# Optimization experiments

Hardware: AMD Instinct MI355X
Metric: run time of the kernel (lower is better)

The kernel has to match this reference:

```python
import jax, jax.numpy as jnp
import numpy as np

B, P, K, E, H, V, C = 128, 64, 64, 300, 300, 50000, 3


def lstm0(x, Wih, bih, bhh):
    # PyTorch LSTMCell single step with zero initial (h, c) state.
    # gates = x @ Wih^T + bih + Whh @ 0 + bhh ; chunks order: i, f, g, o
    g = x @ Wih.T + bih + bhh
    i, f, gg, o = jnp.split(g, 4, axis=-1)
    c = jax.nn.sigmoid(i) * jnp.tanh(gg)
    return jax.nn.sigmoid(o) * jnp.tanh(c)


def setup_inputs() -> dict:
    key = jax.random.key(0)
    ks = jax.random.split(key, 24)
    d = {}
    d["premise"] = jax.random.randint(ks[0], (B, P), 1, V)
    d["premise_len"] = jax.random.randint(ks[1], (B,), P // 2, P + 1)
    d["hypothesis"] = jax.random.randint(ks[2], (B, K), 1, V)
    d["hypothesis_len"] = jax.random.randint(ks[3], (B,), K // 2, K + 1)
    embed = jax.random.normal(ks[4], (V, E), jnp.float32) * 0.1
    d["embed"] = embed.at[0].set(0.0)  # padding_idx=0
    d["w_e"] = jax.random.uniform(ks[5], (H,), jnp.float32)
    xav = (2.0 / (H + H)) ** 0.5
    d["W_s"] = jax.random.normal(ks[6], (H, H), jnp.float32) * xav
    d["W_t"] = jax.random.normal(ks[7], (H, H), jnp.float32) * xav
    d["W_m"] = jax.random.normal(ks[8], (H, H), jnp.float32) * xav
    d["fc_w"] = jax.random.normal(ks[9], (C, H), jnp.float32) * (2.0 / (H + C)) ** 0.5
    d["fc_b"] = jax.random.uniform(ks[10], (C,), jnp.float32)
    s = 1.0 / np.sqrt(H)
    def cell(k1, k2, k3, k4, in_dim):
        return (jax.random.uniform(k1, (4 * H, in_dim), jnp.float32, -s, s),
                jax.random.uniform(k2, (4 * H, H), jnp.float32, -s, s),
                jax.random.uniform(k3, (4 * H,), jnp.float32, -s, s),
                jax.random.uniform(k4, (4 * H,), jnp.float32, -s, s))
    d["Wih_p"], d["Whh_p"], d["bih_p"], d["bhh_p"] = cell(ks[11], ks[12], ks[13], ks[14], E)
    d["Wih_h"], d["Whh_h"], d["bih_h"], d["bhh_h"] = cell(ks[15], ks[16], ks[17], ks[18], E)
    d["Wih_m"], d["Whh_m"], d["bih_m"], d["bhh_m"] = cell(ks[19], ks[20], ks[21], ks[22], 2 * H)
    return d


def reference(premise, premise_len, hypothesis, hypothesis_len, embed, w_e,
              W_s, W_t, W_m, fc_w, fc_b,
              Wih_p, Whh_p, bih_p, bhh_p,
              Wih_h, Whh_h, bih_h, bhh_h,
              Wih_m, Whh_m, bih_m, bhh_m):
    prem_emb = embed[premise]      # [B,P,E]
    hypo_emb = embed[hypothesis]   # [B,K,E]
    # Original code calls LSTMCell on a whole sequence -> per-token single step
    # with zero initial state (no temporal recurrence in these two cells).
    h_s = lstm0(prem_emb, Wih_p, bih_p, bhh_p)  # [B,P,H]
    h_t = lstm0(hypo_emb, Wih_h, bih_h, bhh_h)  # [B,K,H]
    s_proj = h_s @ W_s.T                         # [B,P,H]
    t_proj = jnp.transpose(h_t @ W_t.T, (1, 0, 2))  # [K,B,H]
    h_t_kb = jnp.transpose(h_t, (1, 0, 2))          # [K,B,H]
    b, p = h_s.shape[0], h_s.shape[1]
    pmask = jnp.arange(p)[None, :] < premise_len[:, None]  # [B,P]
    neg = jnp.finfo(s_proj.dtype).min

    def step(h_m, xs):
        t_k, ht_k = xs  # [B,H], [B,H]
        m_proj = h_m @ W_m.T  # [B,H]
        e = jnp.einsum('bph,h->bp',
                       jnp.tanh(s_proj + t_k[:, None, :] + m_proj[:, None, :]), w_e)
        e = jnp.where(pmask, e, neg)
        alpha = jax.nn.softmax(e, axis=1)           # softmax over valid premise pos
        a = jnp.einsum('bp,bph->bh', alpha, h_s)    # attention-weighted premise
        m = jnp.concatenate([a, ht_k], axis=-1)     # [B,2H]
        # lstm_match is re-invoked with zero state each k in the original
        h_m_new = lstm0(m, Wih_m, bih_m, bhh_m)
        return h_m_new, h_m_new

    _, hs_all = jax.lax.scan(step, jnp.zeros((b, s_proj.shape[-1]), s_proj.dtype),
                             (t_proj, h_t_kb))      # [K,B,H]
    h_fin = hs_all[hypothesis_len - 1, jnp.arange(b)]  # h_m at last valid hypo step
    logits = h_fin @ fc_w.T + fc_b
    return jax.nn.softmax(logits, axis=1)
```

## Files before the change

kernel.cpp:

```cpp
#include <hip/hip_runtime.h>
#include <stdint.h>

typedef unsigned short u16;
typedef __attribute__((ext_vector_type(8))) __bf16 bf16x8;
typedef __attribute__((ext_vector_type(4))) float f32x4;

__device__ __forceinline__ float bf2f(u16 u) {
    union { unsigned int i; float f; } v; v.i = ((unsigned int)u) << 16; return v.f;
}
__device__ __forceinline__ float bf2f_lo(unsigned int u) {
    union { unsigned int i; float f; } v; v.i = u << 16; return v.f;
}
__device__ __forceinline__ float bf2f_hi(unsigned int u) {
    union { unsigned int i; float f; } v; v.i = u & 0xffff0000u; return v.f;
}
__device__ __forceinline__ u16 f2bf(float f) {
    union { float f; unsigned int i; } v; v.f = f;
    unsigned int x = v.i;
    unsigned int r = (x + 0x7fffu + ((x >> 16) & 1u)) >> 16;
    return (u16)r;
}
__device__ __forceinline__ float rdf(const void* p, size_t i, int isbf) {
    return isbf ? bf2f(((const u16*)p)[i]) : ((const float*)p)[i];
}
__device__ __forceinline__ float fast_sigmoid(float x) {
    return __builtin_amdgcn_rcpf(1.f + __expf(-x));
}
__device__ __forceinline__ float fast_tanh(float x) {
    float u = __expf(x + x);
    return 1.f - 2.f * __builtin_amdgcn_rcpf(u + 1.f);
}
__device__ __forceinline__ bf16x8 as_bf8(uint4 u) {
    union { uint4 a; bf16x8 b; } c; c.a = u; return c.b;
}

#define BB 128
#define PP 64
#define KK 64
#define HH 300
#define MROWS 8192
#define KPAD 320
#define N3H 900
#define GLD 912
#define NT1 19
#define NT4 57

__global__ void detect_dtype(const u16* __restrict__ raw, int* __restrict__ flag) {
    __shared__ int cnt;
    if (threadIdx.x == 0) cnt = 0;
    __syncthreads();
    if (threadIdx.x < 300 && (raw[threadIdx.x] & 0x8000u)) atomicAdd(&cnt, 1);
    __syncthreads();
    if (threadIdx.x == 0) *flag = (cnt < 8) ? 1 : 0;
}

__global__ void pack_w(const void* __restrict__ src, u16* __restrict__ dst,
                       int dstRowsPad, int nsrcRows, int srcld, int colOff, int igo,
                       const int* __restrict__ flag) {
    int i = blockIdx.x * 256 + threadIdx.x;
    if (i >= dstRowsPad * KPAD) return;
    int isbf = *flag;
    int r = i / KPAD, c = i % KPAD;
    u16 v = 0;
    if (r < nsrcRows && c < HH) {
        int sr = igo ? (r < HH ? r : r + HH) : r;
        v = f2bf(rdf(src, (size_t)sr * srcld + colOff + c, isbf));
    }
    dst[i] = v;
}

__global__ void pack_wf(const void* __restrict__ Wm, uint4* __restrict__ dst,
                        const int* __restrict__ flag) {
    int i = blockIdx.x * 256 + threadIdx.x;
    if (i >= NT1 * 10 * 64) return;
    int isbf = *flag;
    int lane = i & 63, ks = (i >> 6) % 10, T = i / 640;
    int j = T * 16 + (lane & 15);
    int k0 = 32 * ks + 8 * (lane >> 4);
    unsigned int d[4];
    #pragma unroll
    for (int q = 0; q < 4; ++q) {
        int ka = k0 + 2 * q, kb = k0 + 2 * q + 1;
        unsigned int lo = (j < 300 && ka < 300) ? f2bf(rdf(Wm, (size_t)j * HH + ka, isbf)) : 0;
        unsigned int hi = (j < 300 && kb < 300) ? f2bf(rdf(Wm, (size_t)j * HH + kb, isbf)) : 0;
        d[q] = lo | (hi << 16);
    }
    uint4 v; v.x = d[0]; v.y = d[1]; v.z = d[2]; v.w = d[3];
    dst[i] = v;
}

__global__ void pack_bias(const void* bip, const void* bhp, const void* bih_, const void* bhh_,
                          const void* bim, const void* bhm,
                          float* bp, float* bh, float* bm, const int* __restrict__ flag) {
    int i = blockIdx.x * 256 + threadIdx.x;
    if (i >= 3 * N3H) return;
    int isbf = *flag;
    int which = i / N3H, r = i % N3H;
    int sr = (r < HH) ? r : r + HH;
    if (which == 0)      bp[r] = rdf(bip, sr, isbf) + rdf(bhp, sr, isbf);
    else if (which == 1) bh[r] = rdf(bih_, sr, isbf) + rdf(bhh_, sr, isbf);
    else                 bm[r] = rdf(bim, sr, isbf) + rdf(bhm, sr, isbf);
}

__global__ void gather_embed(const int* __restrict__ idx, const void* __restrict__ embed,
                             u16* __restrict__ X, const int* __restrict__ flag) {
    int i = blockIdx.x * 256 + threadIdx.x;
    int isbf = *flag;
    int r = i / KPAD, c = i % KPAD;
    X[i] = (c < HH) ? f2bf(rdf(embed, (size_t)idx[r] * HH + c, isbf)) : (u16)0;
}

__global__ void zero_out(u16* out) { out[threadIdx.x] = 0; }

__global__ __launch_bounds__(256) void gemm_bt(
    const u16* __restrict__ A, const u16* __restrict__ B,
    u16* __restrict__ Cb, const float* __restrict__ bias, int N, int ldc, int frag)
{
    __shared__ __align__(16) u16 At[128 * 32];
    __shared__ __align__(16) u16 Bt[128 * 32];
    const int tid = threadIdx.x;
    const int m0 = blockIdx.x * 128;
    const int n0 = blockIdx.y * 128;
    const int lane = tid & 63;
    const int wave = tid >> 6;
    const int rm = (wave & 1) * 64;
    const int rn = (wave >> 1) * 64;
    const int qr = lane >> 4;
    const int lr = lane & 15;

    f32x4 acc[4][4] = {};

    const int c0 = tid, c1 = tid + 256;
    const int r0 = c0 >> 2, o0 = (c0 & 3) * 8;
    const int r1 = c1 >> 2, o1 = (c1 & 3) * 8;

    for (int k0 = 0; k0 < KPAD; k0 += 32) {
        uint4 a0v = *(const uint4*)(A + (size_t)(m0 + r0) * KPAD + k0 + o0);
        uint4 a1v = *(const uint4*)(A + (size_t)(m0 + r1) * KPAD + k0 + o1);
        uint4 b0v = *(const uint4*)(B + (size_t)(n0 + r0) * KPAD + k0 + o0);
        uint4 b1v = *(const uint4*)(B + (size_t)(n0 + r1) * KPAD + k0 + o1);
        __syncthreads();
        *(uint4*)(At + c0 * 8) = a0v;
        *(uint4*)(At + c1 * 8) = a1v;
        *(uint4*)(Bt + c0 * 8) = b0v;
        *(uint4*)(Bt + c1 * 8) = b1v;
        __syncthreads();
        bf16x8 af[4], bfr[4];
        #pragma unroll
        for (int i = 0; i < 4; ++i) {
            af[i]  = *(const bf16x8*)(At + (rm + i * 16 + lr) * 32 + qr * 8);
            bfr[i] = *(const bf16x8*)(Bt + (rn + i * 16 + lr) * 32 + qr * 8);
        }
        #pragma unroll
        for (int mi = 0; mi < 4; ++mi)
            #pragma unroll
            for (int ni = 0; ni < 4; ++ni)
                acc[mi][ni] = __builtin_amdgcn_mfma_f32_16x16x32_bf16(
                    af[mi], bfr[ni], acc[mi][ni], 0, 0, 0);
    }
    #pragma unroll
    for (int mi = 0; mi < 4; ++mi) {
        #pragma unroll
        for (int ni = 0; ni < 4; ++ni) {
            int n = n0 + rn + ni * 16 + lr;
            int mb = m0 + rm + mi * 16 + qr * 4;
            if (!frag) {
                if (n >= ldc) continue;
                if (n < N) {
                    float bv = bias ? bias[n] : 0.f;
                    #pragma unroll
                    for (int r = 0; r < 4; ++r)
                        Cb[(size_t)(mb + r) * ldc + n] = f2bf(acc[mi][ni][r] + bv);
                } else {
                    #pragma unroll
                    for (int r = 0; r < 4; ++r)
                        Cb[(size_t)(mb + r) * ldc + n] = 0;
                }
            } else {
                if (n >= GLD) continue;
                int bb = mb >> 6, p0 = mb & 63;
                size_t base = ((((size_t)bb * NT4 + (n >> 4)) * 2 + (p0 >> 5)) * 64
                               + ((p0 >> 3) & 3) * 16 + (n & 15)) * 8 + (p0 & 7);
                u16 wv[4];
                if (n < N) {
                    float bv = bias ? bias[n] : 0.f;
                    #pragma unroll
                    for (int r = 0; r < 4; ++r) wv[r] = f2bf(acc[mi][ni][r] + bv);
                } else {
                    #pragma unroll
                    for (int r = 0; r < 4; ++r) wv[r] = 0;
                }
                uint2 st;
                st.x = (unsigned int)wv[0] | ((unsigned int)wv[1] << 16);
                st.y = (unsigned int)wv[2] | ((unsigned int)wv[3] << 16);
                *(uint2*)(Cb + base) = st;
            }
        }
    }
}

__global__ void lstm_act(const u16* __restrict__ gates, u16* __restrict__ hout) {
    int idx = blockIdx.x * 256 + threadIdx.x;
    int r = idx / KPAD, c = idx % KPAD;
    float h = 0.f;
    if (c < HH) {
        const u16* g = gates + (size_t)r * N3H;
        float gi = bf2f(g[c]);
        float gg = bf2f(g[c + HH]);
        float go = bf2f(g[c + 2 * HH]);
        float cc = fast_sigmoid(gi) * fast_tanh(gg);
        h = fast_sigmoid(go) * fast_tanh(cc);
    }
    hout[idx] = f2bf(h);
}

__global__ __launch_bounds__(512)
__attribute__((amdgpu_waves_per_eu(2, 2)))
void scan_kernel(
    const u16* __restrict__ sproj,
    const u16* __restrict__ tproj,
    const uint4* __restrict__ Gmf,
    const u16* __restrict__ hp,
    const uint4* __restrict__ Wf,
    const void* __restrict__ w_e,
    const int* __restrict__ premise_len,
    const int* __restrict__ hypothesis_len,
    float* __restrict__ hfin,
    const int* __restrict__ flag)
{
    __shared__ __align__(16) uint4 gml[NT4 * 2 * 64];
    __shared__ __align__(16) uint4 wlds[3 * 10 * 64];
    __shared__ __align__(16) float we2[320];
    __shared__ __align__(16) float tpm[320];
    __shared__ __align__(16) unsigned int hmhi[160];
    __shared__ __align__(16) unsigned int hmlo[160];
    __shared__ __align__(16) u16 aw[8][128];
    __shared__ float evals[64];
    __shared__ __align__(16) float gates[912];

    const int b = blockIdx.x, t = threadIdx.x;
    const int lane = t & 63, w = t >> 6;
    const int lr = lane & 15, qr = lane >> 4;
    const int plen = premise_len[b], hlen = hypothesis_len[b];
    const int isbf = *flag;

    for (int i = t; i < 3 * 10 * 64; i += 512) wlds[i] = Wf[16 * 640 + i];
    {
        const uint4* gsrc = Gmf + (size_t)b * (NT4 * 2 * 64);
        for (int i = t; i < NT4 * 2 * 64; i += 512) gml[i] = gsrc[i];
    }
    if (t < 320) { we2[t] = (t < 300) ? 2.f * rdf(w_e, t, isbf) : 0.f; tpm[t] = 0.f; }
    if (t < 160) { hmhi[t] = 0; hmlo[t] = 0; }

    uint4 wreg[20];
    #pragma unroll
    for (int ks = 0; ks < 10; ++ks) wreg[ks]      = Wf[(size_t)w * 640 + ks * 64 + lane];
    #pragma unroll
    for (int ks = 0; ks < 10; ++ks) wreg[10 + ks] = Wf[(size_t)(w + 8) * 640 + ks * 64 + lane];

    const int p2p = t >> 3, p2s = t & 7;
    unsigned int spd[20];
    {
        const uint4* sprow = (const uint4*)(sproj + (size_t)(b * PP + p2p) * KPAD + 40 * p2s);
        #pragma unroll
        for (int q = 0; q < 5; ++q) {
            uint4 v = sprow[q];
            spd[4 * q] = v.x; spd[4 * q + 1] = v.y; spd[4 * q + 2] = v.z; spd[4 * q + 3] = v.w;
        }
    }
    __syncthreads();

    float wsum = 0.f;
    #pragma unroll
    for (int q = 0; q < 10; ++q) {
        float4 v = ((const float4*)we2)[10 * p2s + q];
        wsum += 0.5f * ((v.x + v.y) + (v.z + v.w));
    }

    const int nt4 = (w == 0) ? 8 : 7;

    for (int k = 0; k < hlen; ++k) {
        const u16* tprow = tproj + (size_t)(b * KK + k) * KPAD;
        const u16* hprow = hp + (size_t)(b * KK + k) * 900;

        u16 hpv[8];
        #pragma unroll
        for (int i = 0; i < 8; ++i) {
            hpv[i] = 0;
            if (i < nt4 && lane < 16) hpv[i] = hprow[(w + 8 * i) * 16 + lane];
        }
        u16 tk0 = 0, tk1 = 0, tk2 = 0;
        if (lane < 16) {
            tk0 = tprow[w * 16 + lane];
            tk1 = tprow[(w + 8) * 16 + lane];
            if (w < 3) tk2 = tprow[(w + 16) * 16 + lane];
        }

        bf16x8 a1[10];
        {
            const unsigned int* abase = (lr == 1) ? hmlo : hmhi;
            uint4 z; z.x = 0; z.y = 0; z.z = 0; z.w = 0;
            #pragma unroll
            for (int ks = 0; ks < 10; ++ks) {
                uint4 u = *(const uint4*)(abase + 16 * ks + 4 * qr);
                a1[ks] = as_bf8((lr < 2) ? u : z);
            }
        }
        {
            f32x4 aW0 = {}, aW1 = {}, aV0 = {}, aV1 = {};
            #pragma unroll
            for (int ks = 0; ks < 10; ks += 2) {
                aW0 = __builtin_amdgcn_mfma_f32_16x16x32_bf16(a1[ks], as_bf8(wreg[ks]), aW0, 0, 0, 0);
                aV0 = __builtin_amdgcn_mfma_f32_16x16x32_bf16(a1[ks], as_bf8(wreg[10 + ks]), aV0, 0, 0, 0);
                aW1 = __builtin_amdgcn_mfma_f32_16x16x32_bf16(a1[ks + 1], as_bf8(wreg[ks + 1]), aW1, 0, 0, 0);
                aV1 = __builtin_amdgcn_mfma_f32_16x16x32_bf16(a1[ks + 1], as_bf8(wreg[11 + ks]), aV1, 0, 0, 0);
            }
            if (lane < 16) {
                tpm[w * 16 + lane]       = 2.f * (bf2f(tk0) + ((aW0[0] + aW0[1]) + (aW1[0] + aW1[1])));
                tpm[(w + 8) * 16 + lane] = 2.f * (bf2f(tk1) + ((aV0[0] + aV0[1]) + (aV1[0] + aV1[1])));
            }
        }
        if (w < 3) {
            f32x4 ac0 = {}, ac1 = {};
            #pragma unroll
            for (int ks = 0; ks < 10; ks += 2) {
                bf16x8 b0 = as_bf8(wlds[w * 640 + ks * 64 + lane]);
                bf16x8 b1 = as_bf8(wlds[w * 640 + (ks + 1) * 64 + lane]);
                ac0 = __builtin_amdgcn_mfma_f32_16x16x32_bf16(a1[ks], b0, ac0, 0, 0, 0);
                ac1 = __builtin_amdgcn_mfma_f32_16x16x32_bf16(a1[ks + 1], b1, ac1, 0, 0, 0);
            }
            if (lane < 16) tpm[(w + 16) * 16 + lane] = 2.f * (bf2f(tk2) + ((ac0[0] + ac0[1]) + (ac1[0] + ac1[1])));
        }
        __syncthreads();

        {
            float accn = 0.f;
            bool act = p2p < plen;
            if (act) {
                #pragma unroll
                for (int q = 0; q < 10; ++q) {
                    float4 tv = ((const float4*)tpm)[10 * p2s + q];
                    float4 wv = ((const float4*)we2)[10 * p2s + q];
                    float x0 = fmaf(2.f, bf2f_lo(spd[2 * q]), tv.x);
                    float x1 = fmaf(2.f, bf2f_hi(spd[2 * q]), tv.y);
                    float x2 = fmaf(2.f, bf2f_lo(spd[2 * q + 1]), tv.z);
                    float x3 = fmaf(2.f, bf2f_hi(spd[2 * q + 1]), tv.w);
                    accn = fmaf(wv.x, __builtin_amdgcn_rcpf(__expf(x0) + 1.f), accn);
                    accn = fmaf(wv.y, __builtin_amdgcn_rcpf(__expf(x1) + 1.f), accn);
                    accn = fmaf(wv.z, __builtin_amdgcn_rcpf(__expf(x2) + 1.f), accn);
                    accn = fmaf(wv.w, __builtin_amdgcn_rcpf(__expf(x3) + 1.f), accn);
                }
            }
            float val = act ? (wsum - accn) : 0.f;
            val += __shfl_down(val, 4);
            val += __shfl_down(val, 2);
            val += __shfl_down(val, 1);
            if (p2s == 0) evals[p2p] = act ? val : -1e30f;
        }
        __syncthreads();

        {
            float v = evals[lane];
            float mx = v;
            #pragma unroll
            for (int d = 32; d; d >>= 1) mx = fmaxf(mx, __shfl_xor(mx, d));
            float ex = (lane < plen) ? __expf(v - mx) : 0.f;
            float sm = ex;
            #pragma unroll
            for (int d = 32; d; d >>= 1) sm += __shfl_xor(sm, d);
            float al = ex * __builtin_amdgcn_rcpf(sm);
            u16 ah = f2bf(al);
            aw[w][lane] = ah;
            aw[w][64 + lane] = f2bf(al - bf2f(ah));
        }

        bf16x8 a4[2];
        {
            const u16* abase = aw[w] + ((lr == 1) ? 64 : 0);
            uint4 z; z.x = 0; z.y = 0; z.z = 0; z.w = 0;
            #pragma unroll
            for (int ks = 0; ks < 2; ++ks) {
                uint4 u = *(const uint4*)(abase + 32 * ks + 8 * qr);
                a4[ks] = as_bf8((lr < 2) ? u : z);
            }
        }
        #pragma unroll
        for (int i = 0; i < 8; ++i) {
            if (i < nt4) {
                int T = w + 8 * i;
                f32x4 ac0 = {}, ac1 = {};
                ac0 = __builtin_amdgcn_mfma_f32_16x16x32_bf16(a4[0], as_bf8(gml[(T * 2 + 0) * 64 + lane]), ac0, 0, 0, 0);
                ac1 = __builtin_amdgcn_mfma_f32_16x16x32_bf16(a4[1], as_bf8(gml[(T * 2 + 1) * 64 + lane]), ac1, 0, 0, 0);
                if (lane < 16) gates[T * 16 + lane] = ((ac0[0] + ac0[1]) + (ac1[0] + ac1[1])) + bf2f(hpv[i]);
            }
        }
        __syncthreads();

        if (t < 300) {
            float gi = gates[t], gg = gates[300 + t], go = gates[600 + t];
            float cc = fast_sigmoid(gi) * fast_tanh(gg);
            float h = fast_sigmoid(go) * fast_tanh(cc);
            if (k == hlen - 1) hfin[(size_t)b * KPAD + t] = h;
            u16 hh = f2bf(h);
            float res = h - bf2f(hh);
            float hn = __shfl_down(h, 1);
            float rn2 = __shfl_down(res, 1);
            if ((t & 1) == 0) {
                hmhi[t >> 1] = (unsigned int)hh | ((unsigned int)f2bf(hn) << 16);
                hmlo[t >> 1] = (unsigned int)f2bf(res) | ((unsigned int)f2bf(rn2) << 16);
            }
        }
        __syncthreads();
    }
}

__global__ void fc_softmax(const float* __restrict__ hfin, const void* __restrict__ fcw,
                           const void* __restrict__ fcb, void* __restrict__ out,
                           const int* __restrict__ flag) {
    int b = threadIdx.x;
    int isbf = *flag;
    float l[3];
    #pragma unroll
    for (int c = 0; c < 3; ++c) {
        float acc = rdf(fcb, c, isbf);
        const float* hr = hfin + (size_t)b * KPAD;
        for (int h = 0; h < HH; ++h) acc += hr[h] * rdf(fcw, (size_t)c * HH + h, isbf);
        l[c] = acc;
    }
    float mx = fmaxf(l[0], fmaxf(l[1], l[2]));
    float e0 = __expf(l[0] - mx), e1 = __expf(l[1] - mx), e2 = __expf(l[2] - mx);
    float inv = __builtin_amdgcn_rcpf(e0 + e1 + e2);
    if (isbf) {
        u16* o = (u16*)out;
        o[b * 3 + 0] = f2bf(e0 * inv);
        o[b * 3 + 1] = f2bf(e1 * inv);
        o[b * 3 + 2] = f2bf(e2 * inv);
    } else {
        float* o = (float*)out;
        o[b * 3 + 0] = e0 * inv;
        o[b * 3 + 1] = e1 * inv;
        o[b * 3 + 2] = e2 * inv;
    }
}

extern "C" void kernel_launch(void* const* d_in, const int* in_sizes, int n_in,
                              void* d_out, int out_size, void* d_ws, size_t ws_size,
                              hipStream_t stream) {
    const int* premise        = (const int*)d_in[0];
    const int* premise_len    = (const int*)d_in[1];
    const int* hypothesis     = (const int*)d_in[2];
    const int* hypothesis_len = (const int*)d_in[3];
    const void* embed = d_in[4];
    const void* w_e   = d_in[5];
    const void* W_s   = d_in[6];
    const void* W_t   = d_in[7];
    const void* W_m   = d_in[8];
    const void* fc_w  = d_in[9];
    const void* fc_b  = d_in[10];
    const void* Wih_p = d_in[11];
    const void* bih_p = d_in[13];
    const void* bhh_p = d_in[14];
    const void* Wih_h = d_in[15];
    const void* bih_h = d_in[17];
    const void* bhh_h = d_in[18];
    const void* Wih_m = d_in[19];
    const void* bih_m = d_in[21];
    const void* bhh_m = d_in[22];
    (void)in_sizes; (void)n_in; (void)out_size;

    char* w = (char*)d_ws;
    auto alloc = [&](size_t bytes) -> char* {
        char* r = (char*)(((uintptr_t)w + 255) & ~(uintptr_t)255);
        w = r + bytes;
        return r;
    };
    char* regA = alloc((size_t)MROWS * KPAD * 2);
    char* regB = alloc((size_t)MROWS * GLD * 2);
    char* regC = alloc((size_t)MROWS * N3H * 2);
    char* regD = alloc((size_t)MROWS * KPAD * 2);
    char* regE = alloc((size_t)MROWS * KPAD * 2);
    u16* Wp_pad  = (u16*)alloc((size_t)1024 * KPAD * 2);
    u16* Wh_pad  = (u16*)alloc((size_t)1024 * KPAD * 2);
    u16* Wa_pad  = (u16*)alloc((size_t)1024 * KPAD * 2);
    u16* Whm_pad = (u16*)alloc((size_t)1024 * KPAD * 2);
    u16* Ws_pad  = (u16*)alloc((size_t)384 * KPAD * 2);
    u16* Wt_pad  = (u16*)alloc((size_t)384 * KPAD * 2);
    uint4* Wf    = (uint4*)alloc((size_t)NT1 * 10 * 64 * 16);
    float* bsum_p = (float*)alloc(N3H * 4);
    float* bsum_h = (float*)alloc(N3H * 4);
    float* bsum_m = (float*)alloc(N3H * 4);
    int* dflag   = (int*)alloc(256);
    size_t needed = (size_t)(w - (char*)d_ws);
    if (needed > ws_size) {
        zero_out<<<1, 384, 0, stream>>>((u16*)d_out);
        return;
    }
    u16* Xbuf   = (u16*)regA;
    u16* s_proj = (u16*)regA;
    u16* h_s    = (u16*)regD;
    u16* t_proj = (u16*)regD;
    u16* h_t    = (u16*)regE;
    float* h_fin = (float*)regE;

    detect_dtype<<<1, 320, 0, stream>>>((const u16*)w_e, dflag);
    pack_w<<<1280, 256, 0, stream>>>(Wih_p, Wp_pad, 1024, N3H, HH, 0, 1, dflag);
    pack_w<<<1280, 256, 0, stream>>>(Wih_h, Wh_pad, 1024, N3H, HH, 0, 1, dflag);
    pack_w<<<1280, 256, 0, stream>>>(Wih_m, Wa_pad, 1024, N3H, 600, 0, 1, dflag);
    pack_w<<<1280, 256, 0, stream>>>(Wih_m, Whm_pad, 1024, N3H, 600, HH, 1, dflag);
    pack_w<<<480, 256, 0, stream>>>(W_s, Ws_pad, 384, HH, HH, 0, 0, dflag);
    pack_w<<<480, 256, 0, stream>>>(W_t, Wt_pad, 384, HH, HH, 0, 0, dflag);
    pack_wf<<<48, 256, 0, stream>>>(W_m, Wf, dflag);
    pack_bias<<<11, 256, 0, stream>>>(bih_p, bhh_p, bih_h, bhh_h, bih_m, bhh_m,
                                      bsum_p, bsum_h, bsum_m, dflag);

    gather_embed<<<10240, 256, 0, stream>>>(premise, embed, Xbuf, dflag);
    gemm_bt<<<dim3(64, 8), 256, 0, stream>>>(Xbuf, Wp_pad, (u16*)regB, bsum_p, N3H, N3H, 0);
    lstm_act<<<10240, 256, 0, stream>>>((u16*)regB, h_s);
    gather_embed<<<10240, 256, 0, stream>>>(hypothesis, embed, Xbuf, dflag);
    gemm_bt<<<dim3(64, 8), 256, 0, stream>>>(Xbuf, Wh_pad, (u16*)regC, bsum_h, N3H, N3H, 0);
    lstm_act<<<10240, 256, 0, stream>>>((u16*)regC, h_t);

    gemm_bt<<<dim3(64, 3), 256, 0, stream>>>(h_s, Ws_pad, s_proj, nullptr, HH, KPAD, 0);
    gemm_bt<<<dim3(64, 8), 256, 0, stream>>>(h_s, Wa_pad, (u16*)regB, nullptr, N3H, 0, 1);
    gemm_bt<<<dim3(64, 3), 256, 0, stream>>>(h_t, Wt_pad, t_proj, nullptr, HH, KPAD, 0);
    gemm_bt<<<dim3(64, 8), 256, 0, stream>>>(h_t, Whm_pad, (u16*)regC, bsum_m, N3H, N3H, 0);

    scan_kernel<<<BB, 512, 0, stream>>>(s_proj, t_proj, (const uint4*)regB,
                                        (const u16*)regC, Wf, w_e,
                                        premise_len, hypothesis_len, h_fin, dflag);
    fc_softmax<<<1, 128, 0, stream>>>(h_fin, fc_w, fc_b, d_out, dflag);
}
```

Measured before the change: 672.0 us.

## Widen scan kernel to 16 waves and repartition attention work per wave

The sequential scan kernel now runs 1024 threads (16 waves) per batch element instead of 512. Each wave handles one W_m tile and one slice of the hidden dimension for all 64 premise positions. Partial attention sums are reduced through shared memory by wave 0, which also computes the softmax once and shares it, instead of every wave recomputing it. This halves per-thread register state and spreads the serial per-step work over more waves, at the cost of an extra barrier per step and a single-wave reduction/softmax stage.

```diff
diff --git a/kernel.cpp b/kernel.cpp
--- a/kernel.cpp
+++ b/kernel.cpp
@@ -44,6 +44,7 @@
 #define GLD 912
 #define NT1 19
 #define NT4 57
+#define NW 16
 
 __global__ void detect_dtype(const u16* __restrict__ raw, int* __restrict__ flag) {
     __shared__ int cnt;
@@ -100,6 +101,12 @@
     if (which == 0)      bp[r] = rdf(bip, sr, isbf) + rdf(bhp, sr, isbf);
     else if (which == 1) bh[r] = rdf(bih_, sr, isbf) + rdf(bhh_, sr, isbf);
     else                 bm[r] = rdf(bim, sr, isbf) + rdf(bhm, sr, isbf);
+}
+
+__global__ void pack_we(const void* __restrict__ we, float* __restrict__ dst,
+                        const int* __restrict__ flag) {
+    int i = threadIdx.x;
+    dst[i] = (i < 300) ? 2.f * rdf(we, i, *flag) : 0.f;
 }
 
 __global__ void gather_embed(const int* __restrict__ idx, const void* __restrict__ embed,
@@ -214,86 +221,89 @@
     hout[idx] = f2bf(h);
 }
 
-__global__ __launch_bounds__(512)
-__attribute__((amdgpu_waves_per_eu(2, 2)))
-void scan_kernel(
+__global__ __launch_bounds__(1024) void scan_kernel(
     const u16* __restrict__ sproj,
     const u16* __restrict__ tproj,
     const uint4* __restrict__ Gmf,
     const u16* __restrict__ hp,
     const uint4* __restrict__ Wf,
-    const void* __restrict__ w_e,
+    const float* __restrict__ we2g,
     const int* __restrict__ premise_len,
     const int* __restrict__ hypothesis_len,
-    float* __restrict__ hfin,
-    const int* __restrict__ flag)
+    float* __restrict__ hfin)
 {
     __shared__ __align__(16) uint4 gml[NT4 * 2 * 64];
     __shared__ __align__(16) uint4 wlds[3 * 10 * 64];
-    __shared__ __align__(16) float we2[320];
     __shared__ __align__(16) float tpm[320];
     __shared__ __align__(16) unsigned int hmhi[160];
     __shared__ __align__(16) unsigned int hmlo[160];
-    __shared__ __align__(16) u16 aw[8][128];
-    __shared__ float evals[64];
+    __shared__ __align__(16) float part[NW][64];
+    __shared__ __align__(16) u16 aw_sh[128];
     __shared__ __align__(16) float gates[912];
 
     const int b = blockIdx.x, t = threadIdx.x;
     const int lane = t & 63, w = t >> 6;
     const int lr = lane & 15, qr = lane >> 4;
     const int plen = premise_len[b], hlen = hypothesis_len[b];
-    const int isbf = *flag;
-
-    for (int i = t; i < 3 * 10 * 64; i += 512) wlds[i] = Wf[16 * 640 + i];
+
     {
         const uint4* gsrc = Gmf + (size_t)b * (NT4 * 2 * 64);
-        for (int i = t; i < NT4 * 2 * 64; i += 512) gml[i] = gsrc[i];
-    }
-    if (t < 320) { we2[t] = (t < 300) ? 2.f * rdf(w_e, t, isbf) : 0.f; tpm[t] = 0.f; }
+        for (int i = t; i < NT4 * 2 * 64; i += 1024) gml[i] = gsrc[i];
+    }
+    for (int i = t; i < 3 * 10 * 64; i += 1024) wlds[i] = Wf[16 * 640 + i];
+    if (t < 320) tpm[t] = 0.f;
     if (t < 160) { hmhi[t] = 0; hmlo[t] = 0; }
 
-    uint4 wreg[20];
+    uint4 wreg[10];
     #pragma unroll
-    for (int ks = 0; ks < 10; ++ks) wreg[ks]      = Wf[(size_t)w * 640 + ks * 64 + lane];
+    for (int ks = 0; ks < 10; ++ks) wreg[ks] = Wf[(size_t)w * 640 + ks * 64 + lane];
+
+    unsigned int spd[10];
+    {
+        const u16* srow = sproj + (size_t)(b * PP + lane) * KPAD + 20 * w;
+        #pragma unroll
+        for (int q = 0; q < 5; ++q) {
+            uint2 v = *(const uint2*)(srow + 4 * q);
+            spd[2 * q] = v.x; spd[2 * q + 1] = v.y;
+        }
+    }
+    const int wu = __builtin_amdgcn_readfirstlane(w);
+    const float* wep = we2g + 20 * wu;
+    float we_s[20];
     #pragma unroll
-    for (int ks = 0; ks < 10; ++ks) wreg[10 + ks] = Wf[(size_t)(w + 8) * 640 + ks * 64 + lane];
-
-    const int p2p = t >> 3, p2s = t & 7;
-    unsigned int spd[20];
-    {
-        const uint4* sprow = (const uint4*)(sproj + (size_t)(b * PP + p2p) * KPAD + 40 * p2s);
-        #pragma unroll
-        for (int q = 0; q < 5; ++q) {
-            uint4 v = sprow[q];
-            spd[4 * q] = v.x; spd[4 * q + 1] = v.y; spd[4 * q + 2] = v.z; spd[4 * q + 3] = v.w;
-        }
+    for (int j = 0; j < 20; ++j) we_s[j] = wep[j];
+
+    float wsumf = 0.f;
+    if (w == 0) {
+        float s = 0.f;
+        #pragma unroll
+        for (int q = 0; q < 5; ++q) s += we2g[lane + 64 * q];
+        #pragma unroll
+        for (int d = 32; d; d >>= 1) s += __shfl_xor(s, d);
+        wsumf = 0.5f * s;
     }
     __syncthreads();
 
-    float wsum = 0.f;
-    #pragma unroll
-    for (int q = 0; q < 10; ++q) {
-        float4 v = ((const float4*)we2)[10 * p2s + q];
-        wsum += 0.5f * ((v.x + v.y) + (v.z + v.w));
-    }
-
-    const int nt4 = (w == 0) ? 8 : 7;
+    const int nt4 = (w < 9) ? 4 : 3;
+    const bool act2 = lane < plen;
 
     for (int k = 0; k < hlen; ++k) {
         const u16* tprow = tproj + (size_t)(b * KK + k) * KPAD;
         const u16* hprow = hp + (size_t)(b * KK + k) * 900;
 
-        u16 hpv[8];
-        #pragma unroll
-        for (int i = 0; i < 8; ++i) {
+        u16 hpv[4];
+        #pragma unroll
+        for (int i = 0; i < 4; ++i) {
             hpv[i] = 0;
-            if (i < nt4 && lane < 16) hpv[i] = hprow[(w + 8 * i) * 16 + lane];
-        }
-        u16 tk0 = 0, tk1 = 0, tk2 = 0;
+            if (i < nt4 && lane < 16) {
+                int j = (w + 16 * i) * 16 + lane;
+                if (j < 900) hpv[i] = hprow[j];
+            }
+        }
+        u16 tk0 = 0, tk1 = 0;
         if (lane < 16) {
             tk0 = tprow[w * 16 + lane];
-            tk1 = tprow[(w + 8) * 16 + lane];
-            if (w < 3) tk2 = tprow[(w + 16) * 16 + lane];
+            if (w < 3) tk1 = tprow[(16 + w) * 16 + lane];
         }
 
         bf16x8 a1[10];
@@ -307,18 +317,13 @@
             }
         }
         {
-            f32x4 aW0 = {}, aW1 = {}, aV0 = {}, aV1 = {};
+            f32x4 ac0 = {}, ac1 = {};
             #pragma unroll
             for (int ks = 0; ks < 10; ks += 2) {
-                aW0 = __builtin_amdgcn_mfma_f32_16x16x32_bf16(a1[ks], as_bf8(wreg[ks]), aW0, 0, 0, 0);
-                aV0 = __builtin_amdgcn_mfma_f32_16x16x32_bf16(a1[ks], as_bf8(wreg[10 + ks]), aV0, 0, 0, 0);
-                aW1 = __builtin_amdgcn_mfma_f32_16x16x32_bf16(a1[ks + 1], as_bf8(wreg[ks + 1]), aW1, 0, 0, 0);
-                aV1 = __builtin_amdgcn_mfma_f32_16x16x32_bf16(a1[ks + 1], as_bf8(wreg[11 + ks]), aV1, 0, 0, 0);
-            }
-            if (lane < 16) {
-                tpm[w * 16 + lane]       = 2.f * (bf2f(tk0) + ((aW0[0] + aW0[1]) + (aW1[0] + aW1[1])));
-                tpm[(w + 8) * 16 + lane] = 2.f * (bf2f(tk1) + ((aV0[0] + aV0[1]) + (aV1[0] + aV1[1])));
-            }
+                ac0 = __builtin_amdgcn_mfma_f32_16x16x32_bf16(a1[ks], as_bf8(wreg[ks]), ac0, 0, 0, 0);
+                ac1 = __builtin_amdgcn_mfma_f32_16x16x32_bf16(a1[ks + 1], as_bf8(wreg[ks + 1]), ac1, 0, 0, 0);
+            }
+            if (lane < 16) tpm[w * 16 + lane] = 2.f * (bf2f(tk0) + ((ac0[0] + ac0[1]) + (ac1[0] + ac1[1])));
         }
         if (w < 3) {
             f32x4 ac0 = {}, ac1 = {};
@@ -329,54 +334,52 @@
                 ac0 = __builtin_amdgcn_mfma_f32_16x16x32_bf16(a1[ks], b0, ac0, 0, 0, 0);
                 ac1 = __builtin_amdgcn_mfma_f32_16x16x32_bf16(a1[ks + 1], b1, ac1, 0, 0, 0);
             }
-            if (lane < 16) tpm[(w + 16) * 16 + lane] = 2.f * (bf2f(tk2) + ((ac0[0] + ac0[1]) + (ac1[0] + ac1[1])));
+            if (lane < 16) tpm[(16 + w) * 16 + lane] = 2.f * (bf2f(tk1) + ((ac0[0] + ac0[1]) + (ac1[0] + ac1[1])));
         }
         __syncthreads();
 
         {
-            float accn = 0.f;
-            bool act = p2p < plen;
-            if (act) {
+            float accn0 = 0.f, accn1 = 0.f;
+            if (act2) {
                 #pragma unroll
-                for (int q = 0; q < 10; ++q) {
-                    float4 tv = ((const float4*)tpm)[10 * p2s + q];
-                    float4 wv = ((const float4*)we2)[10 * p2s + q];
+                for (int q = 0; q < 5; ++q) {
+                    float4 tv = ((const float4*)tpm)[5 * w + q];
                     float x0 = fmaf(2.f, bf2f_lo(spd[2 * q]), tv.x);
                     float x1 = fmaf(2.f, bf2f_hi(spd[2 * q]), tv.y);
                     float x2 = fmaf(2.f, bf2f_lo(spd[2 * q + 1]), tv.z);
                     float x3 = fmaf(2.f, bf2f_hi(spd[2 * q + 1]), tv.w);
-                    accn = fmaf(wv.x, __builtin_amdgcn_rcpf(__expf(x0) + 1.f), accn);
-                    accn = fmaf(wv.y, __builtin_amdgcn_rcpf(__expf(x1) + 1.f), accn);
-                    accn = fmaf(wv.z, __builtin_amdgcn_rcpf(__expf(x2) + 1.f), accn);
-                    accn = fmaf(wv.w, __builtin_amdgcn_rcpf(__expf(x3) + 1.f), accn);
+                    accn0 = fmaf(we_s[4 * q],     __builtin_amdgcn_rcpf(__expf(x0) + 1.f), accn0);
+                    accn1 = fmaf(we_s[4 * q + 1], __builtin_amdgcn_rcpf(__expf(x1) + 1.f), accn1);
+                    accn0 = fmaf(we_s[4 * q + 2], __builtin_amdgcn_rcpf(__expf(x2) + 1.f), accn0);
+                    accn1 = fmaf(we_s[4 * q + 3], __builtin_amdgcn_rcpf(__expf(x3) + 1.f), accn1);
                 }
             }
-            float val = act ? (wsum - accn) : 0.f;
-            val += __shfl_down(val, 4);
-            val += __shfl_down(val, 2);
-            val += __shfl_down(val, 1);
-            if (p2s == 0) evals[p2p] = act ? val : -1e30f;
-        }
-        __syncthreads();
-
-        {
-            float v = evals[lane];
-            float mx = v;
+            part[w][lane] = act2 ? (accn0 + accn1) : 0.f;
+        }
+        __syncthreads();
+
+        if (w == 0) {
+            float s = 0.f;
+            #pragma unroll
+            for (int q = 0; q < NW; ++q) s += part[q][lane];
+            float e = act2 ? (wsumf - s) : -1e30f;
+            float mx = e;
             #pragma unroll
             for (int d = 32; d; d >>= 1) mx = fmaxf(mx, __shfl_xor(mx, d));
-            float ex = (lane < plen) ? __expf(v - mx) : 0.f;
+            float ex = act2 ? __expf(e - mx) : 0.f;
             float sm = ex;
             #pragma unroll
             for (int d = 32; d; d >>= 1) sm += __shfl_xor(sm, d);
             float al = ex * __builtin_amdgcn_rcpf(sm);
             u16 ah = f2bf(al);
-            aw[w][lane] = ah;
-            aw[w][64 + lane] = f2bf(al - bf2f(ah));
-        }
+            aw_sh[lane] = ah;
+            aw_sh[64 + lane] = f2bf(al - bf2f(ah));
+        }
+        __syncthreads();
 
         bf16x8 a4[2];
         {
-            const u16* abase = aw[w] + ((lr == 1) ? 64 : 0);
+            const u16* abase = aw_sh + ((lr == 1) ? 64 : 0);
             uint4 z; z.x = 0; z.y = 0; z.z = 0; z.w = 0;
             #pragma unroll
             for (int ks = 0; ks < 2; ++ks) {
@@ -385,9 +388,9 @@
             }
         }
         #pragma unroll
-        for (int i = 0; i < 8; ++i) {
+        for (int i = 0; i < 4; ++i) {
             if (i < nt4) {
-                int T = w + 8 * i;
+                int T = w + 16 * i;
                 f32x4 ac0 = {}, ac1 = {};
                 ac0 = __builtin_amdgcn_mfma_f32_16x16x32_bf16(a4[0], as_bf8(gml[(T * 2 + 0) * 64 + lane]), ac0, 0, 0, 0);
                 ac1 = __builtin_amdgcn_mfma_f32_16x16x32_bf16(a4[1], as_bf8(gml[(T * 2 + 1) * 64 + lane]), ac1, 0, 0, 0);
@@ -486,6 +489,7 @@
     u16* Ws_pad  = (u16*)alloc((size_t)384 * KPAD * 2);
     u16* Wt_pad  = (u16*)alloc((size_t)384 * KPAD * 2);
     uint4* Wf    = (uint4*)alloc((size_t)NT1 * 10 * 64 * 16);
+    float* we2g  = (float*)alloc(320 * 4);
     float* bsum_p = (float*)alloc(N3H * 4);
     float* bsum_h = (float*)alloc(N3H * 4);
     float* bsum_m = (float*)alloc(N3H * 4);
@@ -510,6 +514,7 @@
     pack_w<<<480, 256, 0, stream>>>(W_s, Ws_pad, 384, HH, HH, 0, 0, dflag);
     pack_w<<<480, 256, 0, stream>>>(W_t, Wt_pad, 384, HH, HH, 0, 0, dflag);
     pack_wf<<<48, 256, 0, stream>>>(W_m, Wf, dflag);
+    pack_we<<<1, 320, 0, stream>>>(w_e, we2g, dflag);
     pack_bias<<<11, 256, 0, stream>>>(bih_p, bhh_p, bih_h, bhh_h, bih_m, bhh_m,
                                       bsum_p, bsum_h, bsum_m, dflag);
 
@@ -525,8 +530,8 @@
     gemm_bt<<<dim3(64, 3), 256, 0, stream>>>(h_t, Wt_pad, t_proj, nullptr, HH, KPAD, 0);
     gemm_bt<<<dim3(64, 8), 256, 0, stream>>>(h_t, Whm_pad, (u16*)regC, bsum_m, N3H, N3H, 0);
 
-    scan_kernel<<<BB, 512, 0, stream>>>(s_proj, t_proj, (const uint4*)regB,
-                                        (const u16*)regC, Wf, w_e,
-                                        premise_len, hypothesis_len, h_fin, dflag);
+    scan_kernel<<<BB, 1024, 0, stream>>>(s_proj, t_proj, (const uint4*)regB,
+                                         (const u16*)regC, Wf, we2g,
+                                         premise_len, hypothesis_len, h_fin);
     fc_softmax<<<1, 128, 0, stream>>>(h_fin, fc_w, fc_b, d_out, dflag);
 }
```

Result: faster. 642.3 us (-4.4%).
